# Kernel tuning notes

Measured on AMD Instinct MI355X. Metric: run time of the kernel, lower is better.

The kernel has to match this reference:

```python
import jax, jax.numpy as jnp
import numpy as np

E = 65536
MUL0, MUL1 = 32, 16              # multiplicities of 0e and 1o in irreps_in1/out
FC_IN, FC_HID = 64, 64
WNUMEL = MUL0*MUL0 + MUL1*MUL0 + MUL0*MUL1 + MUL1*MUL1  # 2304
SILU_NORM = 1.6790                # e3nn normalize2mom constant for silu
ISQRT3 = float(1.0 / np.sqrt(3.0))  # w3j entries for l<=1 paths


def setup_inputs() -> dict:
    key = jax.random.key(0)
    k1, k2, k3, k4, k5 = jax.random.split(key, 5)
    return {
        "fea_in1": jax.random.normal(k1, (E, MUL0 + 3 * MUL1), jnp.float32),
        "fea_in2": jax.random.normal(k2, (E, 4), jnp.float32),
        "fea_weight": jax.random.normal(k3, (E, FC_IN), jnp.float32),
        "W1": jax.random.normal(k4, (FC_IN, FC_HID), jnp.float32),
        "W2": jax.random.normal(k5, (FC_HID, WNUMEL), jnp.float32),
    }


def reference(fea_in1, fea_in2, fea_weight, W1, W2):
    # --- e3nn FullyConnectedNet: variance-preserving linear + normalized silu ---
    h = SILU_NORM * jax.nn.silu(fea_weight @ (W1 / np.sqrt(FC_IN)))   # [E, FC_HID]
    w = h @ (W2 / np.sqrt(FC_HID))                                    # [E, WNUMEL]

    # --- split generated per-edge weights into the 4 uvw paths ---
    s0 = MUL0 * MUL0
    s1 = s0 + MUL1 * MUL0
    s2 = s1 + MUL0 * MUL1
    w00 = w[:, :s0].reshape(E, MUL0, MUL0)     # 0e x 0e -> 0e
    w110 = w[:, s0:s1].reshape(E, MUL1, MUL0)  # 1o x 1o -> 0e
    w011 = w[:, s1:s2].reshape(E, MUL0, MUL1)  # 0e x 1o -> 1o
    w101 = w[:, s2:].reshape(E, MUL1, MUL1)    # 1o x 0e -> 1o

    # --- split irrep blocks ---
    x1_0 = fea_in1[:, :MUL0]                       # [E, 32]
    x1_1 = fea_in1[:, MUL0:].reshape(E, MUL1, 3)   # [E, 16, 3]
    x2_0 = fea_in2[:, 0]                           # [E]
    x2_1 = fea_in2[:, 1:4]                         # [E, 3]

    # path weights: sqrt(ir_out.dim / (mul_in1*mul_in2 * n_paths_to_output))
    pw00 = float(np.sqrt(1.0 / (MUL0 * 2)))
    pw110 = float(np.sqrt(1.0 / (MUL1 * 2)))
    pw011 = float(np.sqrt(3.0 / (MUL0 * 2)))
    pw101 = float(np.sqrt(3.0 / (MUL1 * 2)))

    # CG contractions (w3j(0,0,0)=1, w3j(1,1,0)=delta/sqrt3, w3j(0,1,1)=w3j(1,0,1)=delta/sqrt3)
    out0 = pw00 * jnp.einsum('eu,e,euw->ew', x1_0, x2_0, w00) \
         + (pw110 * ISQRT3) * jnp.einsum('eui,ei,euw->ew', x1_1, x2_1, w110)   # [E, 32]
    out1 = (pw011 * ISQRT3) * jnp.einsum('eu,ek,euw->ewk', x1_0, x2_1, w011) \
         + (pw101 * ISQRT3) * jnp.einsum('eui,e,euw->ewi', x1_1, x2_0, w101)   # [E, 16, 3]

    return jnp.concatenate([out0, out1.reshape(E, 3 * MUL1)], axis=1)          # [E, 80]
```

## Files before the change

### kernel.cpp

```cpp
#include <hip/hip_runtime.h>
#include <hip/hip_bf16.h>

typedef __attribute__((ext_vector_type(8)))  __bf16 bf16x8;
typedef __attribute__((ext_vector_type(16))) float  f32x16;

#define N_TILES   72
#define W2F_ELEMS (72*4*64*8)
#define W1F_ELEMS (2*4*64*8)

__device__ __forceinline__ void gload_lds16(const void* g, void* l) {
    __builtin_amdgcn_global_load_lds(
        (const __attribute__((address_space(1))) unsigned int*)g,
        (__attribute__((address_space(3))) unsigned int*)l, 16, 0, 0);
}

__device__ __forceinline__ unsigned pk_bf16(float a, float b) {
    unsigned r;
    asm("v_cvt_pk_bf16_f32 %0, %1, %2" : "=v"(r) : "v"(a), "v"(b));
    return r;
}

__global__ __launch_bounds__(256) void equiconv_prep(const float* __restrict__ W1,
                                                     const float* __restrict__ W2,
                                                     __bf16* __restrict__ W1F,
                                                     __bf16* __restrict__ W2F) {
    int idx = blockIdx.x * 256 + threadIdx.x;
    if (idx < W2F_ELEMS) {
        int j  = idx & 7;
        int ln = (idx >> 3) & 63;
        int ks = (idx >> 9) & 3;
        int t  = idx >> 11;
        int m  = 32 * t + (ln & 31);
        int c  = ks * 16 + 8 * (ln >> 5) + j;
        W2F[idx] = (__bf16)(W2[c * 2304 + m] * 0.125f);
    } else {
        int i2 = idx - W2F_ELEMS;
        if (i2 < W1F_ELEMS) {
            int j  = i2 & 7;
            int ln = (i2 >> 3) & 63;
            int ks = (i2 >> 9) & 3;
            int mt = i2 >> 11;
            int c  = 32 * mt + (ln & 31);
            int in = ks * 16 + 8 * (ln >> 5) + j;
            W1F[i2] = (__bf16)(W1[in * 64 + c] * 0.125f);
        }
    }
}

__global__ __launch_bounds__(256, 2) void equiconv_main(const float* __restrict__ fea_in1,
                                                        const float* __restrict__ fea_in2,
                                                        const float* __restrict__ fea_w,
                                                        const __bf16* __restrict__ W2F,
                                                        const __bf16* __restrict__ W1F,
                                                        float* __restrict__ out) {
    __shared__ __align__(16) float smemf[10368];
    __bf16* RING = (__bf16*)smemf;
    char*   rgb  = (char*)smemf;
    const char* w2b = (const char*)W2F;

    const int tid  = threadIdx.x;
    const int lane = tid & 63;
    const int wv   = tid >> 6;
    const int l31  = lane & 31;
    const int hi   = lane >> 5;
    const int eBlk = blockIdx.x * 128;
    const int eLoc = wv * 32 + l31;

#define STAGE(T) {                                                                \
        const char* _s = w2b + ((size_t)(T) << 12) + wv * 1024 + (lane << 4);     \
        char* _d = rgb + (((T) & 7) << 12) + wv * 1024;                           \
        gload_lds16(_s, _d); }

    STAGE(0); STAGE(1); STAGE(2); STAGE(3); STAGE(4); STAGE(5);

    const float* r1 = fea_in1 + (size_t)(eBlk + eLoc) * 80;
    float x10[32];
#pragma unroll
    for (int q = 0; q < 8; ++q) {
        float4 v = *(const float4*)(r1 + 4 * q);
        x10[4 * q] = v.x; x10[4 * q + 1] = v.y; x10[4 * q + 2] = v.z; x10[4 * q + 3] = v.w;
    }
    float x11[48];
#pragma unroll
    for (int q = 0; q < 12; ++q) {
        float4 v = *(const float4*)(r1 + 32 + 4 * q);
        x11[4 * q] = v.x; x11[4 * q + 1] = v.y; x11[4 * q + 2] = v.z; x11[4 * q + 3] = v.w;
    }
    const float4 f2v = *(const float4*)(fea_in2 + (size_t)(eBlk + eLoc) * 4);

    const float c110 = 0.10206207261596577f;
    float cb1[16];
#pragma unroll
    for (int u = 0; u < 16; ++u)
        cb1[u] = c110 * (x11[3 * u] * f2v.y + x11[3 * u + 1] * f2v.z + x11[3 * u + 2] * f2v.w);

    const f32x16 Z16 = {0,0,0,0,0,0,0,0,0,0,0,0,0,0,0,0};
    bf16x8 hfr0, hfr1, hfr2, hfr3;
    {
        bf16x8 bw[4];
        const float* pw = fea_w + (size_t)(eBlk + eLoc) * 64 + hi * 8;
#pragma unroll
        for (int ks = 0; ks < 4; ++ks) {
            float4 u0 = *(const float4*)(pw + ks * 16);
            float4 u1 = *(const float4*)(pw + ks * 16 + 4);
            bf16x8 b;
            b[0] = (__bf16)u0.x; b[1] = (__bf16)u0.y; b[2] = (__bf16)u0.z; b[3] = (__bf16)u0.w;
            b[4] = (__bf16)u1.x; b[5] = (__bf16)u1.y; b[6] = (__bf16)u1.z; b[7] = (__bf16)u1.w;
            bw[ks] = b;
        }
        f32x16 h0 = Z16, h1 = Z16;
#pragma unroll
        for (int ks = 0; ks < 4; ++ks) {
            bf16x8 a0 = *(const bf16x8*)(W1F + (size_t)((0 * 4 + ks) * 64 + lane) * 8);
            h0 = __builtin_amdgcn_mfma_f32_32x32x16_bf16(a0, bw[ks], h0, 0, 0, 0);
            bf16x8 a1 = *(const bf16x8*)(W1F + (size_t)((1 * 4 + ks) * 64 + lane) * 8);
            h1 = __builtin_amdgcn_mfma_f32_32x32x16_bf16(a1, bw[ks], h1, 0, 0, 0);
        }
        float sv[32];
#pragma unroll
        for (int r = 0; r < 16; ++r) {
            float x0 = h0[r];
            sv[r]      = 1.679f * x0 / (1.f + __expf(-x0));
            float x1 = h1[r];
            sv[16 + r] = 1.679f * x1 / (1.f + __expf(-x1));
        }
        uint4 fr[4];
#pragma unroll
        for (int ks = 0; ks < 4; ++ks) {
            const int vb = 8 * ks;
            float oa = hi ? sv[vb + 4] : sv[vb + 0];
            float ob = hi ? sv[vb + 5] : sv[vb + 1];
            float oc = hi ? sv[vb + 6] : sv[vb + 2];
            float od = hi ? sv[vb + 7] : sv[vb + 3];
            float sa = hi ? sv[vb + 0] : sv[vb + 4];
            float sb = hi ? sv[vb + 1] : sv[vb + 5];
            float sc = hi ? sv[vb + 2] : sv[vb + 6];
            float sd = hi ? sv[vb + 3] : sv[vb + 7];
            unsigned o0 = pk_bf16(oa, ob), o1 = pk_bf16(oc, od);
            unsigned s0 = pk_bf16(sa, sb), s1 = pk_bf16(sc, sd);
            unsigned r0 = (unsigned)__shfl_xor((int)s0, 32, 64);
            unsigned r1 = (unsigned)__shfl_xor((int)s1, 32, 64);
            fr[ks].x = hi ? r0 : o0;
            fr[ks].y = hi ? r1 : o1;
            fr[ks].z = hi ? o0 : r0;
            fr[ks].w = hi ? o1 : r1;
        }
        hfr0 = *(bf16x8*)&fr[0];
        hfr1 = *(bf16x8*)&fr[1];
        hfr2 = *(bf16x8*)&fr[2];
        hfr3 = *(bf16x8*)&fr[3];
    }

    const float sA0  = 0.125f * f2v.x;
    const float s101 = 0.17677669529663687f * f2v.x;
    float acc0[16];
    float t011[8];
    float t101[3][8];
#pragma unroll
    for (int r = 0; r < 16; ++r) acc0[r] = 0.f;
#pragma unroll
    for (int s = 0; s < 8; ++s) { t011[s] = 0.f; t101[0][s] = 0.f; t101[1][s] = 0.f; t101[2][s] = 0.f; }

#define WAITV4 asm volatile("s_waitcnt vmcnt(4)" ::: "memory")
#define WAITV2 asm volatile("s_waitcnt vmcnt(2)" ::: "memory")
#define WAITV0 asm volatile("s_waitcnt vmcnt(0)" ::: "memory")

#define EPI_W00(TT) { float cf = sA0 * x10[(TT)];                                 \
        _Pragma("unroll") for (int r = 0; r < 16; ++r) acc0[r] += cf * Cv[r]; }
#define EPI_W110(TT) { float cf = cb1[(TT) - 32];                                 \
        _Pragma("unroll") for (int r = 0; r < 16; ++r) acc0[r] += cf * Cv[r]; }
#define EPI_W011(TT) { const int uu = 2 * ((TT) - 48);                            \
        float cf0 = x10[uu], cf1 = x10[uu + 1];                                   \
        _Pragma("unroll") for (int r = 0; r < 16; ++r)                            \
            t011[r & 7] += (r >= 8 ? cf1 : cf0) * Cv[r]; }
#define EPI_W101(TT) { const int uu = 2 * ((TT) - 64);                            \
        float d00 = x11[3*uu+0],   d01 = x11[3*uu+1],   d02 = x11[3*uu+2];        \
        float d10 = x11[3*uu+3],   d11 = x11[3*uu+4],   d12 = x11[3*uu+5];        \
        _Pragma("unroll") for (int r = 0; r < 16; ++r) { int s = r & 7;           \
            t101[0][s] += (r >= 8 ? d10 : d00) * Cv[r];                           \
            t101[1][s] += (r >= 8 ? d11 : d01) * Cv[r];                           \
            t101[2][s] += (r >= 8 ? d12 : d02) * Cv[r]; } }

#define EPI_ANY(TT) {                                                             \
        if ((TT) < 32)      { EPI_W00(TT) }                                       \
        else if ((TT) < 48) { EPI_W110(TT) }                                      \
        else if ((TT) < 64) { EPI_W011(TT) }                                      \
        else                { EPI_W101(TT) } }

#define DO_TILE(TT) {                                                             \
        const __bf16* tb = RING + (((TT) & 7) << 11) + (lane << 3);               \
        bf16x8 a0 = *(const bf16x8*)(tb);                                         \
        bf16x8 a1 = *(const bf16x8*)(tb + 512);                                   \
        bf16x8 a2 = *(const bf16x8*)(tb + 1024);                                  \
        bf16x8 a3 = *(const bf16x8*)(tb + 1536);                                  \
        f32x16 Cv;                                                                \
        Cv = __builtin_amdgcn_mfma_f32_32x32x16_bf16(a0, hfr0, Z16, 0, 0, 0);     \
        Cv = __builtin_amdgcn_mfma_f32_32x32x16_bf16(a1, hfr1, Cv, 0, 0, 0);      \
        Cv = __builtin_amdgcn_mfma_f32_32x32x16_bf16(a2, hfr2, Cv, 0, 0, 0);      \
        Cv = __builtin_amdgcn_mfma_f32_32x32x16_bf16(a3, hfr3, Cv, 0, 0, 0);      \
        EPI_ANY(TT); }

    WAITV0;

#pragma unroll
    for (int i = 0; i < 36; ++i) {
        if (i < 34)       { WAITV4; }
        else if (i == 34) { WAITV2; }
        else              { WAITV0; }
        __builtin_amdgcn_s_barrier();
        __builtin_amdgcn_sched_barrier(0);
        if (2 * i + 6 < N_TILES) { STAGE(2 * i + 6); STAGE(2 * i + 7); }
        DO_TILE(2 * i);
        DO_TILE(2 * i + 1);
    }

    __syncthreads();
    float* OST = smemf;
#pragma unroll
    for (int r = 0; r < 16; ++r) {
        int rv = (r & 3) + 8 * (r >> 2) + 4 * hi;
        OST[eLoc * 81 + rv] = acc0[r];
    }
#pragma unroll
    for (int s = 0; s < 8; ++s) {
        int w = (s & 3) + 8 * (s >> 2) + 4 * hi;
        float b011 = 0.125f * t011[s];
        OST[eLoc * 81 + 32 + w * 3 + 0] = f2v.y * b011 + s101 * t101[0][s];
        OST[eLoc * 81 + 32 + w * 3 + 1] = f2v.z * b011 + s101 * t101[1][s];
        OST[eLoc * 81 + 32 + w * 3 + 2] = f2v.w * b011 + s101 * t101[2][s];
    }
    __syncthreads();
    {
        float* og = out + (size_t)blockIdx.x * 10240;
        for (int i = tid; i < 10240; i += 256) {
            int el = i / 80;
            int j  = i - el * 80;
            og[i] = OST[el * 81 + j];
        }
    }
}

extern "C" void kernel_launch(void* const* d_in, const int* in_sizes, int n_in,
                              void* d_out, int out_size, void* d_ws, size_t ws_size,
                              hipStream_t stream) {
    const float* fea_in1 = (const float*)d_in[0];
    const float* fea_in2 = (const float*)d_in[1];
    const float* fea_w   = (const float*)d_in[2];
    const float* W1      = (const float*)d_in[3];
    const float* W2      = (const float*)d_in[4];
    __bf16* W2F = (__bf16*)d_ws;
    __bf16* W1F = (__bf16*)((char*)d_ws + (size_t)W2F_ELEMS * 2);

    equiconv_prep<<<(W2F_ELEMS + W1F_ELEMS + 255) / 256, 256, 0, stream>>>(W1, W2, W1F, W2F);
    equiconv_main<<<65536 / 128, 256, 0, stream>>>(fea_in1, fea_in2, fea_w, W2F, W1F, (float*)d_out);
}
```

Before: 112.2 us.

## Move per-edge coefficients to LDS, shrink weight ring, coalesce prep

The per-edge x10/x11 values and the precomputed 1o·1o coefficients now live in a column-major LDS region instead of registers, filled by half the threads. Epilogues read them from LDS, which frees many VGPRs. The W2 tile ring shrinks from 8 to 6 slots with a 4-tile prefetch distance, and a sched_barrier pins the stage issue. The prep kernel is rewritten so each block reads W2 rows with coalesced float4 loads. The trade-offs are extra LDS traffic on every tile, a larger LDS footprint, and a shallower prefetch that can expose load latency.

```diff
diff --git a/kernel.cpp b/kernel.cpp
--- a/kernel.cpp
+++ b/kernel.cpp
@@ -24,18 +24,28 @@
                                                      const float* __restrict__ W2,
                                                      __bf16* __restrict__ W1F,
                                                      __bf16* __restrict__ W2F) {
-    int idx = blockIdx.x * 256 + threadIdx.x;
-    if (idx < W2F_ELEMS) {
-        int j  = idx & 7;
-        int ln = (idx >> 3) & 63;
-        int ks = (idx >> 9) & 3;
-        int t  = idx >> 11;
-        int m  = 32 * t + (ln & 31);
-        int c  = ks * 16 + 8 * (ln >> 5) + j;
-        W2F[idx] = (__bf16)(W2[c * 2304 + m] * 0.125f);
+    const int b = blockIdx.x;
+    const int tid = threadIdx.x;
+    if (b < 72) {
+        const int c   = tid >> 2;
+        const int grp = tid & 3;
+        const float* src = W2 + (size_t)c * 2304 + 32 * b + 8 * grp;
+        float4 u0 = *(const float4*)src;
+        float4 u1 = *(const float4*)(src + 4);
+        const int ks  = c >> 4;
+        const int hib = (c >> 3) & 1;
+        const int j   = c & 7;
+        __bf16* dst = W2F + ((size_t)(b * 4 + ks) * 64 + 32 * hib + 8 * grp) * 8 + j;
+        dst[0 * 8] = (__bf16)(u0.x * 0.125f);
+        dst[1 * 8] = (__bf16)(u0.y * 0.125f);
+        dst[2 * 8] = (__bf16)(u0.z * 0.125f);
+        dst[3 * 8] = (__bf16)(u0.w * 0.125f);
+        dst[4 * 8] = (__bf16)(u1.x * 0.125f);
+        dst[5 * 8] = (__bf16)(u1.y * 0.125f);
+        dst[6 * 8] = (__bf16)(u1.z * 0.125f);
+        dst[7 * 8] = (__bf16)(u1.w * 0.125f);
     } else {
-        int i2 = idx - W2F_ELEMS;
-        if (i2 < W1F_ELEMS) {
+        for (int i2 = tid; i2 < W1F_ELEMS; i2 += 256) {
             int j  = i2 & 7;
             int ln = (i2 >> 3) & 63;
             int ks = (i2 >> 9) & 3;
@@ -47,13 +57,15 @@
     }
 }
 
+#define CFld(c) smemf[6144 + (c) * 128 + eLoc]
+
 __global__ __launch_bounds__(256, 2) void equiconv_main(const float* __restrict__ fea_in1,
                                                         const float* __restrict__ fea_in2,
                                                         const float* __restrict__ fea_w,
                                                         const __bf16* __restrict__ W2F,
                                                         const __bf16* __restrict__ W1F,
                                                         float* __restrict__ out) {
-    __shared__ __align__(16) float smemf[10368];
+    __shared__ __align__(16) float smemf[18432];
     __bf16* RING = (__bf16*)smemf;
     char*   rgb  = (char*)smemf;
     const char* w2b = (const char*)W2F;
@@ -68,31 +80,42 @@
 
 #define STAGE(T) {                                                                \
         const char* _s = w2b + ((size_t)(T) << 12) + wv * 1024 + (lane << 4);     \
-        char* _d = rgb + (((T) & 7) << 12) + wv * 1024;                           \
+        char* _d = rgb + (((T) % 6) << 12) + wv * 1024;                           \
         gload_lds16(_s, _d); }
 
-    STAGE(0); STAGE(1); STAGE(2); STAGE(3); STAGE(4); STAGE(5);
-
-    const float* r1 = fea_in1 + (size_t)(eBlk + eLoc) * 80;
-    float x10[32];
-#pragma unroll
-    for (int q = 0; q < 8; ++q) {
-        float4 v = *(const float4*)(r1 + 4 * q);
-        x10[4 * q] = v.x; x10[4 * q + 1] = v.y; x10[4 * q + 2] = v.z; x10[4 * q + 3] = v.w;
-    }
-    float x11[48];
-#pragma unroll
-    for (int q = 0; q < 12; ++q) {
-        float4 v = *(const float4*)(r1 + 32 + 4 * q);
-        x11[4 * q] = v.x; x11[4 * q + 1] = v.y; x11[4 * q + 2] = v.z; x11[4 * q + 3] = v.w;
-    }
+    STAGE(0); STAGE(1); STAGE(2); STAGE(3);
+
+    if (tid < 128) {
+        const float* r1 = fea_in1 + (size_t)(eBlk + tid) * 80;
+#pragma unroll
+        for (int q = 0; q < 8; ++q) {
+            float4 v = *(const float4*)(r1 + 4 * q);
+            smemf[6144 + (4 * q + 0) * 128 + tid] = v.x;
+            smemf[6144 + (4 * q + 1) * 128 + tid] = v.y;
+            smemf[6144 + (4 * q + 2) * 128 + tid] = v.z;
+            smemf[6144 + (4 * q + 3) * 128 + tid] = v.w;
+        }
+        float xv[48];
+#pragma unroll
+        for (int q = 0; q < 12; ++q) {
+            float4 v = *(const float4*)(r1 + 32 + 4 * q);
+            xv[4 * q + 0] = v.x; xv[4 * q + 1] = v.y; xv[4 * q + 2] = v.z; xv[4 * q + 3] = v.w;
+            smemf[6144 + (48 + 4 * q + 0) * 128 + tid] = v.x;
+            smemf[6144 + (48 + 4 * q + 1) * 128 + tid] = v.y;
+            smemf[6144 + (48 + 4 * q + 2) * 128 + tid] = v.z;
+            smemf[6144 + (48 + 4 * q + 3) * 128 + tid] = v.w;
+        }
+        const float4 f2o = *(const float4*)(fea_in2 + (size_t)(eBlk + tid) * 4);
+        const float c110 = 0.10206207261596577f;
+#pragma unroll
+        for (int u = 0; u < 16; ++u)
+            smemf[6144 + (32 + u) * 128 + tid] =
+                c110 * (xv[3 * u] * f2o.y + xv[3 * u + 1] * f2o.z + xv[3 * u + 2] * f2o.w);
+    }
+
     const float4 f2v = *(const float4*)(fea_in2 + (size_t)(eBlk + eLoc) * 4);
-
-    const float c110 = 0.10206207261596577f;
-    float cb1[16];
-#pragma unroll
-    for (int u = 0; u < 16; ++u)
-        cb1[u] = c110 * (x11[3 * u] * f2v.y + x11[3 * u + 1] * f2v.z + x11[3 * u + 2] * f2v.w);
+    const float sA0  = 0.125f * f2v.x;
+    const float s101 = 0.17677669529663687f * f2v.x;
 
     const f32x16 Z16 = {0,0,0,0,0,0,0,0,0,0,0,0,0,0,0,0};
     bf16x8 hfr0, hfr1, hfr2, hfr3;
@@ -151,8 +174,6 @@
         hfr3 = *(bf16x8*)&fr[3];
     }
 
-    const float sA0  = 0.125f * f2v.x;
-    const float s101 = 0.17677669529663687f * f2v.x;
     float acc0[16];
     float t011[8];
     float t101[3][8];
@@ -161,21 +182,20 @@
 #pragma unroll
     for (int s = 0; s < 8; ++s) { t011[s] = 0.f; t101[0][s] = 0.f; t101[1][s] = 0.f; t101[2][s] = 0.f; }
 
-#define WAITV4 asm volatile("s_waitcnt vmcnt(4)" ::: "memory")
 #define WAITV2 asm volatile("s_waitcnt vmcnt(2)" ::: "memory")
 #define WAITV0 asm volatile("s_waitcnt vmcnt(0)" ::: "memory")
 
-#define EPI_W00(TT) { float cf = sA0 * x10[(TT)];                                 \
+#define EPI_W00(TT) { float cf = sA0 * CFld(TT);                                  \
         _Pragma("unroll") for (int r = 0; r < 16; ++r) acc0[r] += cf * Cv[r]; }
-#define EPI_W110(TT) { float cf = cb1[(TT) - 32];                                 \
+#define EPI_W110(TT) { float cf = CFld(TT);              \
         _Pragma("unroll") for (int r = 0; r < 16; ++r) acc0[r] += cf * Cv[r]; }
 #define EPI_W011(TT) { const int uu = 2 * ((TT) - 48);                            \
-        float cf0 = x10[uu], cf1 = x10[uu + 1];                                   \
+        float cf0 = CFld(uu), cf1 = CFld(uu + 1);                                 \
         _Pragma("unroll") for (int r = 0; r < 16; ++r)                            \
             t011[r & 7] += (r >= 8 ? cf1 : cf0) * Cv[r]; }
-#define EPI_W101(TT) { const int uu = 2 * ((TT) - 64);                            \
-        float d00 = x11[3*uu+0],   d01 = x11[3*uu+1],   d02 = x11[3*uu+2];        \
-        float d10 = x11[3*uu+3],   d11 = x11[3*uu+4],   d12 = x11[3*uu+5];        \
+#define EPI_W101(TT) { const int dd = 48 + 6 * ((TT) - 64);                       \
+        float d00 = CFld(dd + 0), d01 = CFld(dd + 1), d02 = CFld(dd + 2);         \
+        float d10 = CFld(dd + 3), d11 = CFld(dd + 4), d12 = CFld(dd + 5);         \
         _Pragma("unroll") for (int r = 0; r < 16; ++r) { int s = r & 7;           \
             t101[0][s] += (r >= 8 ? d10 : d00) * Cv[r];                           \
             t101[1][s] += (r >= 8 ? d11 : d01) * Cv[r];                           \
@@ -188,7 +208,7 @@
         else                { EPI_W101(TT) } }
 
 #define DO_TILE(TT) {                                                             \
-        const __bf16* tb = RING + (((TT) & 7) << 11) + (lane << 3);               \
+        const __bf16* tb = RING + (((TT) % 6) << 11) + (lane << 3);               \
         bf16x8 a0 = *(const bf16x8*)(tb);                                         \
         bf16x8 a1 = *(const bf16x8*)(tb + 512);                                   \
         bf16x8 a2 = *(const bf16x8*)(tb + 1024);                                  \
@@ -200,16 +220,15 @@
         Cv = __builtin_amdgcn_mfma_f32_32x32x16_bf16(a3, hfr3, Cv, 0, 0, 0);      \
         EPI_ANY(TT); }
 
-    WAITV0;
+    __syncthreads();
 
 #pragma unroll
     for (int i = 0; i < 36; ++i) {
-        if (i < 34)       { WAITV4; }
-        else if (i == 34) { WAITV2; }
-        else              { WAITV0; }
+        if (i < 35) { WAITV2; } else { WAITV0; }
         __builtin_amdgcn_s_barrier();
         __builtin_amdgcn_sched_barrier(0);
-        if (2 * i + 6 < N_TILES) { STAGE(2 * i + 6); STAGE(2 * i + 7); }
+        if (2 * i + 4 < N_TILES) { STAGE(2 * i + 4); STAGE(2 * i + 5); }
+        __builtin_amdgcn_sched_barrier(0);
         DO_TILE(2 * i);
         DO_TILE(2 * i + 1);
     }
@@ -251,6 +270,6 @@
     __bf16* W2F = (__bf16*)d_ws;
     __bf16* W1F = (__bf16*)((char*)d_ws + (size_t)W2F_ELEMS * 2);
 
-    equiconv_prep<<<(W2F_ELEMS + W1F_ELEMS + 255) / 256, 256, 0, stream>>>(W1, W2, W1F, W2F);
+    equiconv_prep<<<73, 256, 0, stream>>>(W1, W2, W1F, W2F);
     equiconv_main<<<65536 / 128, 256, 0, stream>>>(fea_in1, fea_in2, fea_w, W2F, W1F, (float*)d_out);
 }
```

New measurement: 159.8 us. 42.4% more time.
